# Kernel tuning notes

Hardware: AMD Instinct MI355X
Metric: run time of the kernel (lower is better)

## Reference

```python
import jax, jax.numpy as jnp
import numpy as np

B, K, D = 8, 2048, 1024

def setup_inputs() -> dict:
    key = jax.random.key(0)
    k1, k2 = jax.random.split(key)
    x = jax.random.normal(k1, (B, K, D), dtype=jnp.float32)
    W = jax.random.normal(k2, (K, K), dtype=jnp.float32) * 0.02  # dt_proj weight [out=K, in=K]
    b = jnp.zeros((K,), dtype=jnp.float32)                        # dt_proj bias
    return {"x": x, "W": W, "b": b}

def _scan_combine(c1, c2):
    # compose affine maps s -> a*s + u; (a1,u1) then (a2,u2)
    a1, u1 = c1
    a2, u2 = c2
    return (a2 * a1, a2 * u1 + u2)

def reference(x, W, b):
    # lam[b,t,d] = sigmoid( sum_k x[b,k,d] * W[t,k] + b[t] )
    # (dt_proj is a Linear over the TIME axis after permute(0,2,1))
    lam = jax.nn.sigmoid(jnp.einsum('bkd,tk->btd', x, W) + b[None, :, None])
    # s_t = lam_t * s_{t-1} + (1 - lam_t) * x_t, s_0 = 0  -> associative scan over time
    _, ys = jax.lax.associative_scan(_scan_combine, (lam, (1.0 - lam) * x), axis=1)
    return ys
```

## Files before the change

### kernel.cpp

```cpp
#include <hip/hip_runtime.h>
#include <hip/hip_bf16.h>
#include <stdint.h>

#define B_ 8
#define K_ 2048
#define D_ 1024
#define NC 32
#define TC (K_ / NC)

typedef float v4f __attribute__((ext_vector_type(4)));
typedef short v8s __attribute__((ext_vector_type(8)));

__device__ __forceinline__ unsigned short f2bf(float f) {
    __hip_bfloat16 h = __float2bfloat16(f);
    return *reinterpret_cast<unsigned short*>(&h);
}

__device__ __forceinline__ void async_ld16(const void* g, void* l) {
    __builtin_amdgcn_global_load_lds(
        (__attribute__((address_space(1))) void*)(void*)g,
        (__attribute__((address_space(3))) void*)l,
        16, 0, 0);
}

__global__ void conv_w(const float* __restrict__ W, unsigned short* __restrict__ Wb) {
    int i = (blockIdx.x * 256 + threadIdx.x) * 4;
    float4 v = *(const float4*)(W + i);
    ushort4 o;
    o.x = f2bf(v.x); o.y = f2bf(v.y); o.z = f2bf(v.z); o.w = f2bf(v.w);
    *(ushort4*)(Wb + i) = o;
}

__global__ void conv_x_t(const float* __restrict__ x, unsigned short* __restrict__ xT) {
    const int k0 = blockIdx.x * 64, d0 = blockIdx.y * 64, bb = blockIdx.z;
    __shared__ unsigned short tile[64][68];
    const int tid = threadIdx.x;
    const int tx = tid & 15, ty = tid >> 4;
    const float* xp = x + (size_t)bb * K_ * D_;
#pragma unroll
    for (int r = 0; r < 4; r++) {
        int row = ty + r * 16;
        float4 v = *(const float4*)(xp + (size_t)(k0 + row) * D_ + d0 + tx * 4);
        tile[row][tx * 4 + 0] = f2bf(v.x);
        tile[row][tx * 4 + 1] = f2bf(v.y);
        tile[row][tx * 4 + 2] = f2bf(v.z);
        tile[row][tx * 4 + 3] = f2bf(v.w);
    }
    __syncthreads();
    unsigned short* op = xT + (size_t)bb * D_ * K_;
#pragma unroll
    for (int r = 0; r < 4; r++) {
        int dcol = ty + r * 16;
        ushort4 u;
        u.x = tile[tx * 4 + 0][dcol];
        u.y = tile[tx * 4 + 1][dcol];
        u.z = tile[tx * 4 + 2][dcol];
        u.w = tile[tx * 4 + 3][dcol];
        *(ushort4*)(op + (size_t)(d0 + dcol) * K_ + k0 + tx * 4) = u;
    }
}

__launch_bounds__(512, 2)
__global__ void gemm_sig(const unsigned short* __restrict__ Wb,
                         const unsigned short* __restrict__ xT,
                         const float* __restrict__ bias,
                         const float* __restrict__ xf,
                         float* __restrict__ lam,
                         float* __restrict__ Ac,
                         float* __restrict__ Uc,
                         int fuse) {
    __shared__ __align__(16) unsigned short smem_all[2][2][2][256 * 32];

    const int bid = blockIdx.x;
    const int lid = (bid & 7) * 32 + (bid >> 3);
    const int bb = lid >> 5;
    const int tM = (lid >> 2) & 7;
    const int tN = lid & 3;

    const int tid = threadIdx.x;
    const int w = tid >> 6;
    const int lane = tid & 63;
    const int wm = w >> 2;
    const int wn = w & 3;
    const int quad = lane >> 4;
    const int l16 = lane & 15;

    const unsigned short* Ag = Wb + (size_t)(tM * 256) * K_;
    const unsigned short* Bg = xT + (size_t)bb * D_ * K_ + (size_t)(tN * 256) * K_;

    const int srow = lane >> 2;
    const int sgk8 = ((lane & 3) ^ ((lane >> 3) & 3)) * 8;

    const int frg = (quad ^ ((l16 >> 1) & 3)) * 8;
    const int aoff = (wm * 128 + l16) * 32 + frg;
    const int boff = (wn * 64 + l16) * 32 + frg;

    v4f acc[8][4];
#pragma unroll
    for (int i = 0; i < 8; i++)
#pragma unroll
        for (int j = 0; j < 4; j++) acc[i][j] = (v4f)0.f;

#define STAGE_(op, bufi, kh, kk, Gp)                                                        \
    do {                                                                                    \
        async_ld16(Gp + (size_t)(w * 16 + srow) * K_ + (kk) + (kh) * 32 + sgk8,             \
                   &smem_all[op][bufi][kh][w * 512]);                                       \
        async_ld16(Gp + (size_t)((8 + w) * 16 + srow) * K_ + (kk) + (kh) * 32 + sgk8,       \
                   &smem_all[op][bufi][kh][(8 + w) * 512]);                                 \
    } while (0)

    STAGE_(0, 0, 0, 0, Ag);
    STAGE_(1, 0, 0, 0, Bg);
    STAGE_(0, 0, 1, 0, Ag);
    STAGE_(1, 0, 1, 0, Bg);
    asm volatile("s_waitcnt vmcnt(4)");
    asm volatile("s_barrier" ::: "memory");

    v8s af[8], bf[2];

    for (int t = 0; t < K_ / 64; ++t) {
        const int cur = t & 1, nxt = cur ^ 1;
        int k1 = (t + 1) * 64;
        if (k1 == K_) k1 = 0;

#pragma unroll
        for (int i = 0; i < 8; i++) af[i] = *(const v8s*)(&smem_all[0][cur][0][aoff + i * 512]);
        bf[0] = *(const v8s*)(&smem_all[1][cur][0][boff]);
        bf[1] = *(const v8s*)(&smem_all[1][cur][0][boff + 512]);
        STAGE_(0, nxt, 0, k1, Ag);
        asm volatile("s_barrier" ::: "memory");
        asm volatile("s_waitcnt lgkmcnt(0)");
        __builtin_amdgcn_sched_barrier(0);
        __builtin_amdgcn_s_setprio(1);
#pragma unroll
        for (int i = 0; i < 8; i++) {
            acc[i][0] = __builtin_amdgcn_mfma_f32_16x16x32_bf16(af[i], bf[0], acc[i][0], 0, 0, 0);
            acc[i][1] = __builtin_amdgcn_mfma_f32_16x16x32_bf16(af[i], bf[1], acc[i][1], 0, 0, 0);
        }
        __builtin_amdgcn_s_setprio(0);
        asm volatile("s_barrier" ::: "memory");

        bf[0] = *(const v8s*)(&smem_all[1][cur][0][boff + 2 * 512]);
        bf[1] = *(const v8s*)(&smem_all[1][cur][0][boff + 3 * 512]);
        STAGE_(1, nxt, 0, k1, Bg);
        asm volatile("s_barrier" ::: "memory");
        asm volatile("s_waitcnt lgkmcnt(0)");
        __builtin_amdgcn_sched_barrier(0);
        __builtin_amdgcn_s_setprio(1);
#pragma unroll
        for (int i = 0; i < 8; i++) {
            acc[i][2] = __builtin_amdgcn_mfma_f32_16x16x32_bf16(af[i], bf[0], acc[i][2], 0, 0, 0);
            acc[i][3] = __builtin_amdgcn_mfma_f32_16x16x32_bf16(af[i], bf[1], acc[i][3], 0, 0, 0);
        }
        __builtin_amdgcn_s_setprio(0);
        asm volatile("s_waitcnt vmcnt(4)");
        asm volatile("s_barrier" ::: "memory");

#pragma unroll
        for (int i = 0; i < 8; i++) af[i] = *(const v8s*)(&smem_all[0][cur][1][aoff + i * 512]);
        bf[0] = *(const v8s*)(&smem_all[1][cur][1][boff]);
        bf[1] = *(const v8s*)(&smem_all[1][cur][1][boff + 512]);
        STAGE_(0, nxt, 1, k1, Ag);
        asm volatile("s_barrier" ::: "memory");
        asm volatile("s_waitcnt lgkmcnt(0)");
        __builtin_amdgcn_sched_barrier(0);
        __builtin_amdgcn_s_setprio(1);
#pragma unroll
        for (int i = 0; i < 8; i++) {
            acc[i][0] = __builtin_amdgcn_mfma_f32_16x16x32_bf16(af[i], bf[0], acc[i][0], 0, 0, 0);
            acc[i][1] = __builtin_amdgcn_mfma_f32_16x16x32_bf16(af[i], bf[1], acc[i][1], 0, 0, 0);
        }
        __builtin_amdgcn_s_setprio(0);
        asm volatile("s_barrier" ::: "memory");

        bf[0] = *(const v8s*)(&smem_all[1][cur][1][boff + 2 * 512]);
        bf[1] = *(const v8s*)(&smem_all[1][cur][1][boff + 3 * 512]);
        STAGE_(1, nxt, 1, k1, Bg);
        asm volatile("s_barrier" ::: "memory");
        asm volatile("s_waitcnt lgkmcnt(0)");
        __builtin_amdgcn_sched_barrier(0);
        __builtin_amdgcn_s_setprio(1);
#pragma unroll
        for (int i = 0; i < 8; i++) {
            acc[i][2] = __builtin_amdgcn_mfma_f32_16x16x32_bf16(af[i], bf[0], acc[i][2], 0, 0, 0);
            acc[i][3] = __builtin_amdgcn_mfma_f32_16x16x32_bf16(af[i], bf[1], acc[i][3], 0, 0, 0);
        }
        __builtin_amdgcn_s_setprio(0);
        asm volatile("s_waitcnt vmcnt(4)");
        asm volatile("s_barrier" ::: "memory");
    }
#undef STAGE_

    asm volatile("s_waitcnt vmcnt(0)");
    asm volatile("s_barrier" ::: "memory");

    float* out = lam + (size_t)bb * K_ * D_;
    const int dg = tN * 256 + wn * 64;

    if (fuse) {
        float* Swp = (float*)smem_all + w * 4096;
        const int swzw = quad * 16;
#pragma unroll
        for (int cg = 0; cg < 2; cg++) {
            const int c = tM * 4 + wm * 2 + cg;
            const int t0 = c * 64;
#pragma unroll
            for (int ii = 0; ii < 4; ii++) {
                int i = cg * 4 + ii;
                int rowb = t0 + ii * 16 + quad * 4;
                int Rb = ii * 16 + quad * 4;
#pragma unroll
                for (int r = 0; r < 4; r++) {
                    float bt = bias[rowb + r];
#pragma unroll
                    for (int j = 0; j < 4; j++) {
                        int colc = j * 16 + l16;
                        float v = acc[i][j][r] + bt;
                        float sg = 1.f / (1.f + __expf(-v));
                        out[(size_t)(rowb + r) * D_ + dg + colc] = sg;
                        Swp[(Rb + r) * 64 + (colc ^ swzw)] = sg;
                    }
                }
            }
            asm volatile("s_waitcnt lgkmcnt(0)");
            __builtin_amdgcn_sched_barrier(0);
            const float* xg = xf + ((size_t)bb * K_ + t0) * D_ + dg + lane;
            float A = 1.f, U = 0.f;
#pragma unroll 8
            for (int tt = 0; tt < 64; tt++) {
                float l = Swp[tt * 64 + (lane ^ (((tt >> 2) & 3) * 16))];
                float xv = xg[(size_t)tt * D_];
                A *= l;
                U = l * U + (1.f - l) * xv;
            }
            size_t oi = ((size_t)bb * NC + c) * D_ + dg + lane;
            Ac[oi] = A;
            Uc[oi] = U;
            __builtin_amdgcn_sched_barrier(0);
        }
    } else {
#pragma unroll
        for (int i = 0; i < 8; i++) {
            int rowb = tM * 256 + wm * 128 + i * 16 + quad * 4;
#pragma unroll
            for (int r = 0; r < 4; r++) {
                float bt = bias[rowb + r];
#pragma unroll
                for (int j = 0; j < 4; j++) {
                    int col = tN * 256 + wn * 64 + j * 16 + l16;
                    float v = acc[i][j][r] + bt;
                    out[(size_t)(rowb + r) * D_ + col] = 1.f / (1.f + __expf(-v));
                }
            }
        }
    }
}

__global__ void scan_pass1(const float* __restrict__ lam, const float* __restrict__ x,
                           float* __restrict__ Ac, float* __restrict__ Uc) {
    int id = blockIdx.x * 256 + threadIdx.x;
    int d2 = (id & 511) * 2;
    int c = (id >> 9) & (NC - 1);
    int bb = id >> 14;
    const float* lp = lam + ((size_t)bb * K_ + (size_t)c * TC) * D_ + d2;
    const float* xp = x   + ((size_t)bb * K_ + (size_t)c * TC) * D_ + d2;
    float2 A = make_float2(1.f, 1.f), U = make_float2(0.f, 0.f);
#pragma unroll 8
    for (int t = 0; t < TC; t++) {
        float2 l  = *(const float2*)(lp + (size_t)t * D_);
        float2 xv = *(const float2*)(xp + (size_t)t * D_);
        A.x *= l.x; A.y *= l.y;
        U.x = l.x * U.x + (1.f - l.x) * xv.x;
        U.y = l.y * U.y + (1.f - l.y) * xv.y;
    }
    size_t oi = ((size_t)bb * NC + c) * D_ + d2;
    *(float2*)(Ac + oi) = A;
    *(float2*)(Uc + oi) = U;
}

__global__ void scan_pass2(const float* __restrict__ Ac, const float* __restrict__ Uc,
                           float* __restrict__ Sin) {
    int id = blockIdx.x * 64 + threadIdx.x;
    int d = id & (D_ - 1);
    int bb = id >> 10;
    float s = 0.f;
#pragma unroll
    for (int c = 0; c < NC; c++) {
        int idx = (bb * NC + c) * D_ + d;
        Sin[idx] = s;
        s = Ac[idx] * s + Uc[idx];
    }
}

__global__ void scan_pass3(const float* __restrict__ x, const float* __restrict__ Sin,
                           float* __restrict__ lamout) {
    int id = blockIdx.x * 256 + threadIdx.x;
    int d2 = (id & 511) * 2;
    int c = (id >> 9) & (NC - 1);
    int bb = id >> 14;
    float* lp = lamout + ((size_t)bb * K_ + (size_t)c * TC) * D_ + d2;
    const float* xp = x + ((size_t)bb * K_ + (size_t)c * TC) * D_ + d2;
    size_t si = ((size_t)bb * NC + c) * D_ + d2;
    float2 s = *(const float2*)(Sin + si);
#pragma unroll 8
    for (int t = 0; t < TC; t++) {
        float2 l  = *(const float2*)(lp + (size_t)t * D_);
        float2 xv = *(const float2*)(xp + (size_t)t * D_);
        s.x = l.x * s.x + (1.f - l.x) * xv.x;
        s.y = l.y * s.y + (1.f - l.y) * xv.y;
        *(float2*)(lp + (size_t)t * D_) = s;
    }
}

extern "C" void kernel_launch(void* const* d_in, const int* in_sizes, int n_in,
                              void* d_out, int out_size, void* d_ws, size_t ws_size,
                              hipStream_t stream) {
    const float* x    = (const float*)d_in[0];
    const float* W    = (const float*)d_in[1];
    const float* bias = (const float*)d_in[2];
    float* out = (float*)d_out;
    char* ws = (char*)d_ws;

    unsigned short* xT = (unsigned short*)ws;
    unsigned short* Wb = (unsigned short*)(ws + 33554432);

    const int fuse = (ws_size >= 44040192u) ? 1 : 0;
    float* Ac, * Uc;
    if (fuse) {
        Ac = (float*)(ws + 41943040);
        Uc = (float*)(ws + 41943040 + 1048576);
    } else {
        Ac = (float*)(ws + 33554432);
        Uc = (float*)(ws + 33554432 + 1048576);
    }
    float* Sin = (float*)(ws + 33554432 + 2097152);

    conv_w<<<dim3(K_ * K_ / 4 / 256), 256, 0, stream>>>(W, Wb);
    conv_x_t<<<dim3(K_ / 64, D_ / 64, B_), 256, 0, stream>>>(x, xT);
    gemm_sig<<<dim3(256), dim3(512), 0, stream>>>(Wb, xT, bias, x, out, Ac, Uc, fuse);
    if (!fuse)
        scan_pass1<<<dim3(B_ * NC * D_ / 2 / 256), 256, 0, stream>>>(out, x, Ac, Uc);
    scan_pass2<<<dim3(B_ * D_ / 64), 64, 0, stream>>>(Ac, Uc, Sin);
    scan_pass3<<<dim3(B_ * NC * D_ / 2 / 256), 256, 0, stream>>>(x, Sin, out);
}
```

Before: 237.5 us.

## Peel last GEMM iteration, prefetch x in fused scan, merge scan passes 2 and 3

Peels the final k-iteration of the GEMM main loop, so it no longer issues a wasted wrap-around prefetch of tile 0 before the epilogue. In the fused epilogue, all 64 x values are loaded into registers before the LDS wait, so global latency overlaps the lambda writes. Removes the separate scan_pass2 kernel: each scan_pass3 thread now recomputes its chunk's incoming state by serially combining the previous chunk summaries, and processes float4 instead of float2. This saves one launch and the Sin round trip, at the cost of redundant carry recomputation (up to 31 steps), fewer threads, and higher register pressure from the 64-element x array.

After: 237.1 us. About the same (-0.2%).

```diff
diff --git a/kernel.cpp b/kernel.cpp
--- a/kernel.cpp
+++ b/kernel.cpp
@@ -118,10 +118,10 @@
 
     v8s af[8], bf[2];
 
-    for (int t = 0; t < K_ / 64; ++t) {
+    const int NT = K_ / 64;
+    for (int t = 0; t < NT - 1; ++t) {
         const int cur = t & 1, nxt = cur ^ 1;
-        int k1 = (t + 1) * 64;
-        if (k1 == K_) k1 = 0;
+        const int k1 = (t + 1) * 64;
 
 #pragma unroll
         for (int i = 0; i < 8; i++) af[i] = *(const v8s*)(&smem_all[0][cur][0][aoff + i * 512]);
@@ -189,10 +189,68 @@
         asm volatile("s_waitcnt vmcnt(4)");
         asm volatile("s_barrier" ::: "memory");
     }
+
+    {
+        const int cur = (NT - 1) & 1;
+#pragma unroll
+        for (int i = 0; i < 8; i++) af[i] = *(const v8s*)(&smem_all[0][cur][0][aoff + i * 512]);
+        bf[0] = *(const v8s*)(&smem_all[1][cur][0][boff]);
+        bf[1] = *(const v8s*)(&smem_all[1][cur][0][boff + 512]);
+        asm volatile("s_barrier" ::: "memory");
+        asm volatile("s_waitcnt lgkmcnt(0)");
+        __builtin_amdgcn_sched_barrier(0);
+        __builtin_amdgcn_s_setprio(1);
+#pragma unroll
+        for (int i = 0; i < 8; i++) {
+            acc[i][0] = __builtin_amdgcn_mfma_f32_16x16x32_bf16(af[i], bf[0], acc[i][0], 0, 0, 0);
+            acc[i][1] = __builtin_amdgcn_mfma_f32_16x16x32_bf16(af[i], bf[1], acc[i][1], 0, 0, 0);
+        }
+        __builtin_amdgcn_s_setprio(0);
+        asm volatile("s_barrier" ::: "memory");
+
+        bf[0] = *(const v8s*)(&smem_all[1][cur][0][boff + 2 * 512]);
+        bf[1] = *(const v8s*)(&smem_all[1][cur][0][boff + 3 * 512]);
+        asm volatile("s_barrier" ::: "memory");
+        asm volatile("s_waitcnt lgkmcnt(0)");
+        __builtin_amdgcn_sched_barrier(0);
+        __builtin_amdgcn_s_setprio(1);
+#pragma unroll
+        for (int i = 0; i < 8; i++) {
+            acc[i][2] = __builtin_amdgcn_mfma_f32_16x16x32_bf16(af[i], bf[0], acc[i][2], 0, 0, 0);
+            acc[i][3] = __builtin_amdgcn_mfma_f32_16x16x32_bf16(af[i], bf[1], acc[i][3], 0, 0, 0);
+        }
+        __builtin_amdgcn_s_setprio(0);
+        asm volatile("s_waitcnt vmcnt(0)");
+        asm volatile("s_barrier" ::: "memory");
+
+#pragma unroll
+        for (int i = 0; i < 8; i++) af[i] = *(const v8s*)(&smem_all[0][cur][1][aoff + i * 512]);
+        bf[0] = *(const v8s*)(&smem_all[1][cur][1][boff]);
+        bf[1] = *(const v8s*)(&smem_all[1][cur][1][boff + 512]);
+        asm volatile("s_waitcnt lgkmcnt(0)");
+        __builtin_amdgcn_sched_barrier(0);
+        __builtin_amdgcn_s_setprio(1);
+#pragma unroll
+        for (int i = 0; i < 8; i++) {
+            acc[i][0] = __builtin_amdgcn_mfma_f32_16x16x32_bf16(af[i], bf[0], acc[i][0], 0, 0, 0);
+            acc[i][1] = __builtin_amdgcn_mfma_f32_16x16x32_bf16(af[i], bf[1], acc[i][1], 0, 0, 0);
+        }
+        __builtin_amdgcn_s_setprio(0);
+
+        bf[0] = *(const v8s*)(&smem_all[1][cur][1][boff + 2 * 512]);
+        bf[1] = *(const v8s*)(&smem_all[1][cur][1][boff + 3 * 512]);
+        asm volatile("s_waitcnt lgkmcnt(0)");
+        __builtin_amdgcn_sched_barrier(0);
+        __builtin_amdgcn_s_setprio(1);
+#pragma unroll
+        for (int i = 0; i < 8; i++) {
+            acc[i][2] = __builtin_amdgcn_mfma_f32_16x16x32_bf16(af[i], bf[0], acc[i][2], 0, 0, 0);
+            acc[i][3] = __builtin_amdgcn_mfma_f32_16x16x32_bf16(af[i], bf[1], acc[i][3], 0, 0, 0);
+        }
+        __builtin_amdgcn_s_setprio(0);
+        asm volatile("s_barrier" ::: "memory");
+    }
 #undef STAGE_
-
-    asm volatile("s_waitcnt vmcnt(0)");
-    asm volatile("s_barrier" ::: "memory");
 
     float* out = lam + (size_t)bb * K_ * D_;
     const int dg = tN * 256 + wn * 64;
@@ -222,16 +280,19 @@
                     }
                 }
             }
+            const float* xg = xf + ((size_t)bb * K_ + t0) * D_ + dg + lane;
+            float xv[64];
+#pragma unroll
+            for (int tt = 0; tt < 64; tt++) xv[tt] = xg[(size_t)tt * D_];
+
             asm volatile("s_waitcnt lgkmcnt(0)");
             __builtin_amdgcn_sched_barrier(0);
-            const float* xg = xf + ((size_t)bb * K_ + t0) * D_ + dg + lane;
             float A = 1.f, U = 0.f;
-#pragma unroll 8
+#pragma unroll
             for (int tt = 0; tt < 64; tt++) {
                 float l = Swp[tt * 64 + (lane ^ (((tt >> 2) & 3) * 16))];
-                float xv = xg[(size_t)tt * D_];
                 A *= l;
-                U = l * U + (1.f - l) * xv;
+                U = l * U + (1.f - l) * xv[tt];
             }
             size_t oi = ((size_t)bb * NC + c) * D_ + dg + lane;
             Ac[oi] = A;
@@ -278,37 +339,34 @@
     *(float2*)(Uc + oi) = U;
 }
 
-__global__ void scan_pass2(const float* __restrict__ Ac, const float* __restrict__ Uc,
-                           float* __restrict__ Sin) {
-    int id = blockIdx.x * 64 + threadIdx.x;
-    int d = id & (D_ - 1);
-    int bb = id >> 10;
-    float s = 0.f;
-#pragma unroll
-    for (int c = 0; c < NC; c++) {
-        int idx = (bb * NC + c) * D_ + d;
-        Sin[idx] = s;
-        s = Ac[idx] * s + Uc[idx];
-    }
-}
-
-__global__ void scan_pass3(const float* __restrict__ x, const float* __restrict__ Sin,
+__global__ void scan_pass3(const float* __restrict__ x,
+                           const float* __restrict__ Ac, const float* __restrict__ Uc,
                            float* __restrict__ lamout) {
     int id = blockIdx.x * 256 + threadIdx.x;
-    int d2 = (id & 511) * 2;
-    int c = (id >> 9) & (NC - 1);
-    int bb = id >> 14;
-    float* lp = lamout + ((size_t)bb * K_ + (size_t)c * TC) * D_ + d2;
-    const float* xp = x + ((size_t)bb * K_ + (size_t)c * TC) * D_ + d2;
-    size_t si = ((size_t)bb * NC + c) * D_ + d2;
-    float2 s = *(const float2*)(Sin + si);
+    int d = (id & 255) * 4;
+    int c = (id >> 8) & (NC - 1);
+    int bb = id >> 13;
+    float4 s = make_float4(0.f, 0.f, 0.f, 0.f);
+    for (int j = 0; j < c; j++) {
+        size_t ji = ((size_t)bb * NC + j) * D_ + d;
+        float4 A = *(const float4*)(Ac + ji);
+        float4 U = *(const float4*)(Uc + ji);
+        s.x = A.x * s.x + U.x;
+        s.y = A.y * s.y + U.y;
+        s.z = A.z * s.z + U.z;
+        s.w = A.w * s.w + U.w;
+    }
+    float* lp = lamout + ((size_t)bb * K_ + (size_t)c * TC) * D_ + d;
+    const float* xp = x + ((size_t)bb * K_ + (size_t)c * TC) * D_ + d;
 #pragma unroll 8
     for (int t = 0; t < TC; t++) {
-        float2 l  = *(const float2*)(lp + (size_t)t * D_);
-        float2 xv = *(const float2*)(xp + (size_t)t * D_);
+        float4 l  = *(const float4*)(lp + (size_t)t * D_);
+        float4 xv = *(const float4*)(xp + (size_t)t * D_);
         s.x = l.x * s.x + (1.f - l.x) * xv.x;
         s.y = l.y * s.y + (1.f - l.y) * xv.y;
-        *(float2*)(lp + (size_t)t * D_) = s;
+        s.z = l.z * s.z + (1.f - l.z) * xv.z;
+        s.w = l.w * s.w + (1.f - l.w) * xv.w;
+        *(float4*)(lp + (size_t)t * D_) = s;
     }
 }
 
@@ -333,13 +391,11 @@
         Ac = (float*)(ws + 33554432);
         Uc = (float*)(ws + 33554432 + 1048576);
     }
-    float* Sin = (float*)(ws + 33554432 + 2097152);
 
     conv_w<<<dim3(K_ * K_ / 4 / 256), 256, 0, stream>>>(W, Wb);
     conv_x_t<<<dim3(K_ / 64, D_ / 64, B_), 256, 0, stream>>>(x, xT);
     gemm_sig<<<dim3(256), dim3(512), 0, stream>>>(Wb, xT, bias, x, out, Ac, Uc, fuse);
     if (!fuse)
         scan_pass1<<<dim3(B_ * NC * D_ / 2 / 256), 256, 0, stream>>>(out, x, Ac, Uc);
-    scan_pass2<<<dim3(B_ * D_ / 64), 64, 0, stream>>>(Ac, Uc, Sin);
-    scan_pass3<<<dim3(B_ * NC * D_ / 2 / 256), 256, 0, stream>>>(x, Sin, out);
-}
+    scan_pass3<<<dim3(B_ * NC * D_ / 4 / 256), 256, 0, stream>>>(x, Ac, Uc, out);
+}
```
